# Optimization experiments

Measured on AMD Instinct MI355X. Metric: run time of the kernel, lower is better.

The kernel has to match this reference:

```python
import jax, jax.numpy as jnp
import numpy as np

DIM = 256
HEADS = 4
HEAD_DIM = DIM // HEADS
SCALE = HEAD_DIM ** -0.5


def setup_inputs() -> dict:
    key = jax.random.key(0)
    ks = jax.random.split(key, 6)
    B, N, C = 4, 2048, DIM
    t2_grad = jax.random.normal(ks[0], (B, N, C), dtype=jnp.float32)
    t1 = jax.random.normal(ks[1], (B, N, C), dtype=jnp.float32)
    # Linear weights stored as (in, out) so y = x @ W
    Wq = jax.random.normal(ks[2], (C, C), dtype=jnp.float32) * (C ** -0.5)
    Wkv = jax.random.normal(ks[3], (C, 2 * C), dtype=jnp.float32) * (C ** -0.5)
    Wproj = jax.random.normal(ks[4], (C, C), dtype=jnp.float32) * (C ** -0.5)
    bproj = jax.random.normal(ks[5], (C,), dtype=jnp.float32) * 0.01
    gamma = jnp.zeros((1,), dtype=jnp.float32)
    return {"t2_grad": t2_grad, "t1": t1, "Wq": Wq, "Wkv": Wkv,
            "Wproj": Wproj, "bproj": bproj, "gamma": gamma}


def lam(x, gamma):
    # x: (B, H, N, d) -> channel attention over d
    B, H, N, d = x.shape
    xp = jnp.transpose(x, (0, 3, 1, 2))            # (B, d, H, N)
    flat = xp.reshape(B, d, H * N)                 # (B, d, H*N)
    energy = jnp.einsum('bdm,bem->bde', flat, flat)  # (B, d, d)
    # Original applies softmax to raw energy (energy_new is discarded)
    attention = jax.nn.softmax(energy, axis=-1)
    out = jnp.einsum('bde,bem->bdm', attention, flat).reshape(B, d, H, N)
    out = gamma[0] * out + xp
    return jnp.transpose(out, (0, 2, 3, 1))        # (B, H, N, d)


def reference(t2_grad, t1, Wq, Wkv, Wproj, bproj, gamma):
    B, N, C = t2_grad.shape
    H, d = HEADS, HEAD_DIM
    q = (t2_grad @ Wq).reshape(B, N, H, d).transpose(0, 2, 1, 3)      # (B,H,N,d)
    kv = (t1 @ Wkv).reshape(B, N, 2, H, d).transpose(2, 0, 3, 1, 4)   # (2,B,H,N,d)
    k, v = kv[0], kv[1]
    attn = jax.nn.softmax(jnp.einsum('bhnd,bhmd->bhnm', q, k) * SCALE, axis=-1)
    x_other = jnp.einsum('bhnm,bhmd->bhnd', attn, v)                  # (B,H,N,d)
    x_other = lam(x_other, gamma)
    x_other = x_other.transpose(0, 2, 1, 3).reshape(B, N, C) \
        + q.transpose(0, 2, 1, 3).reshape(B, N, C)
    x = t2_grad + x_other
    return x @ Wproj + bproj
```

## Files before the change

kernel.cpp:

```cpp
#include <hip/hip_runtime.h>
#include <hip/hip_bf16.h>


typedef __attribute__((ext_vector_type(8))) short short8_t;
typedef __attribute__((ext_vector_type(4))) float f32x4;
typedef __attribute__((ext_vector_type(2))) unsigned u32x2;

#define NSEQ 2048

static __device__ __forceinline__ short f2bf(float f) {
  union { float f; unsigned u; } v; v.f = f;
  unsigned u = v.u;
  unsigned r = (u + 0x7FFFu + ((u >> 16) & 1u)) >> 16;
  return (short)r;
}
static __device__ __forceinline__ float bf2f(short s) {
  union { unsigned u; float f; } v;
  v.u = ((unsigned)(unsigned short)s) << 16;
  return v.f;
}
static __device__ __forceinline__ unsigned bcu(float f) {
  return __builtin_bit_cast(unsigned, f);
}
static __device__ __forceinline__ unsigned pkbf(float lo, float hi) {
  return __builtin_amdgcn_perm(bcu(hi), bcu(lo), 0x07060302u);
}
static __device__ __forceinline__ short f2bf_hw(float f) {
  __hip_bfloat16 h = __float2bfloat16(f);
  return __builtin_bit_cast(short, h);
}
static __device__ __forceinline__ unsigned pk2bf_hw(float a, float b) {
  return ((unsigned)(unsigned short)__builtin_bit_cast(short, __float2bfloat16(b)) << 16) |
         (unsigned short)__builtin_bit_cast(short, __float2bfloat16(a));
}
static __device__ __forceinline__ f32x4 vmax4(f32x4 a, f32x4 b) {
  f32x4 r;
  r[0] = fmaxf(a[0], b[0]); r[1] = fmaxf(a[1], b[1]);
  r[2] = fmaxf(a[2], b[2]); r[3] = fmaxf(a[3], b[3]);
  return r;
}

static __device__ __forceinline__ void gload_lds16(const short* src, short* ldst) {
  __builtin_amdgcn_global_load_lds(
      (const __attribute__((address_space(1))) unsigned*)src,
      (__attribute__((address_space(3))) unsigned*)ldst, 16, 0, 0);
}

__global__ __launch_bounds__(256) void wconv(
    const float* __restrict__ Wq, const float* __restrict__ Wkv,
    const float* __restrict__ Wp, short* __restrict__ Wqt,
    short* __restrict__ Wkvt, short* __restrict__ Wpt) {
  int tid = blockIdx.x * 256 + threadIdx.x;
  if (tid < 65536) {
    int n = tid >> 8, k = tid & 255;
    Wqt[tid] = f2bf(Wq[k * 256 + n]);
  } else if (tid < 196608) {
    int i = tid - 65536;
    int n = i >> 8, k = i & 255;
    Wkvt[i] = f2bf(Wkv[k * 512 + n]);
  } else {
    int i = tid - 196608;
    int n = i >> 8, k = i & 255;
    Wpt[i] = f2bf(Wp[k * 256 + n]);
  }
}

__global__ __launch_bounds__(256) void gemm_qkv3(
    const float* __restrict__ t2, const float* __restrict__ t1,
    const short* __restrict__ Wqt, const short* __restrict__ Wkvt,
    short* __restrict__ Qb, short* __restrict__ Kb, short* __restrict__ Vtb) {
  __shared__ __align__(16) short ldsA[32 * 256];
  int tid = threadIdx.x;
  int m0 = blockIdx.x * 32;
  int y = blockIdx.y;
  const float* A = (y == 0) ? t2 : t1;

  const float* ap = A + (size_t)m0 * 256;
#pragma unroll
  for (int i = 0; i < 8; i++) {
    int idx = i * 256 + tid;
    int row = idx >> 6, c4 = idx & 63;
    f32x4 v = *(const f32x4*)(ap + (size_t)idx * 4);
    int ch8 = c4 >> 1, half = c4 & 1;
    int swz = ch8 ^ (row & 7);
    unsigned* dst = (unsigned*)&ldsA[row * 256 + swz * 8 + half * 4];
    dst[0] = pk2bf_hw(v[0], v[1]);
    dst[1] = pk2bf_hw(v[2], v[3]);
  }
  __syncthreads();

  int w = tid >> 6, l = tid & 63, lr = l & 15, lg = l >> 4;
  short8_t af[2][8];
#pragma unroll
  for (int mt = 0; mt < 2; mt++)
#pragma unroll
    for (int ks = 0; ks < 8; ks++)
      af[mt][ks] = *(const short8_t*)&ldsA[(mt * 16 + lr) * 256 +
                                           (((ks * 4 + lg) ^ (lr & 7)) * 8)];

  const short* Bt = (y == 0) ? Wqt : (y == 1 ? Wkvt : Wkvt + 65536);
  f32x4 acc[2][4] = {};
#pragma unroll
  for (int ct = 0; ct < 4; ct++) {
    const short* br = Bt + (size_t)(w * 64 + ct * 16 + lr) * 256 + lg * 8;
    short8_t bfr[8];
#pragma unroll
    for (int ks = 0; ks < 8; ks++) bfr[ks] = *(const short8_t*)(br + ks * 32);
    if (y < 2) {
#pragma unroll
      for (int ks = 0; ks < 8; ks++) {
        acc[0][ct] = __builtin_amdgcn_mfma_f32_16x16x32_bf16(af[0][ks], bfr[ks], acc[0][ct], 0, 0, 0);
        acc[1][ct] = __builtin_amdgcn_mfma_f32_16x16x32_bf16(af[1][ks], bfr[ks], acc[1][ct], 0, 0, 0);
      }
    } else {
#pragma unroll
      for (int ks = 0; ks < 8; ks++) {
        acc[0][ct] = __builtin_amdgcn_mfma_f32_16x16x32_bf16(bfr[ks], af[0][ks], acc[0][ct], 0, 0, 0);
        acc[1][ct] = __builtin_amdgcn_mfma_f32_16x16x32_bf16(bfr[ks], af[1][ks], acc[1][ct], 0, 0, 0);
      }
    }
  }
  if (y < 2) {
    short* Ob = (y == 0) ? Qb : Kb;
#pragma unroll
    for (int ct = 0; ct < 4; ct++) {
      int c = w * 64 + ct * 16 + lr;
      int h = c >> 6, dd = c & 63;
#pragma unroll
      for (int mt = 0; mt < 2; mt++)
#pragma unroll
        for (int r = 0; r < 4; r++) {
          int m = m0 + mt * 16 + lg * 4 + r;
          int bb = m >> 11, n = m & 2047;
          Ob[(size_t)(((bb << 2) + h) * NSEQ + n) * 64 + dd] =
              f2bf_hw(acc[mt][ct][r]);
        }
    }
  } else {
#pragma unroll
    for (int ct = 0; ct < 4; ct++) {
      int c = w * 64 + ct * 16 + lg * 4;
#pragma unroll
      for (int mt = 0; mt < 2; mt++) {
        int m = m0 + mt * 16 + lr;
        int bb = m >> 11, n = m & 2047;
#pragma unroll
        for (int r = 0; r < 4; r++) {
          int cc = c + r;
          int h = cc >> 6, dd = cc & 63;
          Vtb[(size_t)(((bb << 2) + h) * 64 + dd) * NSEQ + n] =
              f2bf_hw(acc[mt][ct][r]);
        }
      }
    }
  }
}

template <int NS>
__global__ __launch_bounds__(256, 4) void flash_attn_split(
    const short* __restrict__ Qb, const short* __restrict__ Kb,
    const short* __restrict__ Vt, short* __restrict__ O0,
    short* __restrict__ O1, short* __restrict__ O2,
    short* __restrict__ O3, float* __restrict__ ML) {
  constexpr int KITER = 32 / NS;
  __shared__ __align__(16) short ldsK[2][4096];
  __shared__ __align__(16) short ldsV[4096];
  __shared__ __align__(16) short ldsP[4][2048];
  int tid = threadIdx.x;
  int w = tid >> 6, l = tid & 63, lr = l & 15, lg = l >> 4;
  int bh = blockIdx.y;
  int qt = blockIdx.x / NS, split = blockIdx.x % NS;
  int q0 = qt * 128 + w * 32;
  const short* qpA = Qb + ((size_t)bh * NSEQ + q0 + lr) * 64 + lg * 8;
  const short* qpB = qpA + 16 * 64;
  short8_t qfA0 = *(const short8_t*)qpA;
  short8_t qfA1 = *(const short8_t*)(qpA + 32);
  short8_t qfB0 = *(const short8_t*)qpB;
  short8_t qfB1 = *(const short8_t*)(qpB + 32);
  const short* kbase = Kb + (size_t)bh * NSEQ * 64;
  const short* vbase = Vt + (size_t)bh * 64 * NSEQ;

  int r0 = tid >> 3, ch0 = (tid & 7) ^ (r0 & 7);
  int kb0 = split * KITER;
  const short* ksrc = kbase + (size_t)kb0 * 4096 + (size_t)r0 * 64 + ch0 * 8;
  const short* vsrc = vbase + (size_t)r0 * NSEQ + kb0 * 64 + ch0 * 8;
  short* ldKw0 = &ldsK[0][0] + w * 512;
  short* ldKw1 = &ldsK[1][0] + w * 512;
  short* ldVw = &ldsV[0] + w * 512;

#define STAGE_K(dst_, it_)                                  \
  {                                                         \
    const short* s_ = ksrc + (size_t)(it_) * 4096;          \
    gload_lds16(s_, dst_);                                  \
    gload_lds16(s_ + 2048, (dst_) + 2048);                  \
  }
#define STAGE_V(it_)                                        \
  {                                                         \
    const short* s_ = vsrc + (size_t)(it_) * 64;            \
    gload_lds16(s_, ldVw);                                  \
    gload_lds16(s_ + 32 * NSEQ, ldVw + 2048);               \
  }

  f32x4 oA[4] = {}, oB[4] = {};
  float osumA = 0.f, osumB = 0.f, m2A = -1e30f, m2B = -1e30f;
  const float C = 0.125f * 1.44269504089f;

  int sw = lr & 7;
  int rdA = (lg ^ sw) * 8;
  int rdB = ((lg + 4) ^ sw) * 8;
  short* Pw = &ldsP[w][0];
  short* wrA = Pw + lr * 64 + (lg & 1) * 4;
  short* wrB = wrA + 16 * 64;
  int chhi = lg >> 1;
  const short* prA0 = Pw + lr * 64 + (lg ^ sw) * 8;
  const short* prA1 = Pw + lr * 64 + ((4 + lg) ^ sw) * 8;
  const short* prB0 = prA0 + 16 * 64;
  const short* prB1 = prA1 + 16 * 64;

  STAGE_K(ldKw0, 0);

  for (int i = 0; i < KITER; i++) {
    asm volatile("s_waitcnt vmcnt(0)" ::: "memory");
    __builtin_amdgcn_s_barrier();
    STAGE_V(i);
    if (i + 1 < KITER) {
      short* d_ = (i & 1) ? ldKw0 : ldKw1;
      STAGE_K(d_, i + 1);
    }
    const short* lK = (i & 1) ? &ldsK[1][0] : &ldsK[0][0];
    f32x4 sA[4], sB[4];
    __builtin_amdgcn_s_setprio(1);
#pragma unroll
    for (int t = 0; t < 4; t++) {
      const short* kr = lK + (t * 16 + lr) * 64;
      short8_t kf0 = *(const short8_t*)(kr + rdA);
      short8_t kf1 = *(const short8_t*)(kr + rdB);
      f32x4 z = {0.f, 0.f, 0.f, 0.f};
      f32x4 zA = __builtin_amdgcn_mfma_f32_16x16x32_bf16(kf0, qfA0, z, 0, 0, 0);
      sA[t] = __builtin_amdgcn_mfma_f32_16x16x32_bf16(kf1, qfA1, zA, 0, 0, 0);
      f32x4 zB = __builtin_amdgcn_mfma_f32_16x16x32_bf16(kf0, qfB0, z, 0, 0, 0);
      sB[t] = __builtin_amdgcn_mfma_f32_16x16x32_bf16(kf1, qfB1, zB, 0, 0, 0);
    }
    __builtin_amdgcn_s_setprio(0);
    f32x4 mA4 = vmax4(vmax4(sA[0], sA[1]), vmax4(sA[2], sA[3]));
    f32x4 mB4 = vmax4(vmax4(sB[0], sB[1]), vmax4(sB[2], sB[3]));
    float mxA = fmaxf(fmaxf(mA4[0], mA4[1]), fmaxf(mA4[2], mA4[3]));
    float mxB = fmaxf(fmaxf(mB4[0], mB4[1]), fmaxf(mB4[2], mB4[3]));
    mxA = fmaxf(mxA, __shfl_xor(mxA, 16));
    mxA = fmaxf(mxA, __shfl_xor(mxA, 32));
    mxB = fmaxf(mxB, __shfl_xor(mxB, 16));
    mxB = fmaxf(mxB, __shfl_xor(mxB, 32));
    mxA *= C;
    mxB *= C;
    float mnA = fmaxf(m2A, mxA), mnB = fmaxf(m2B, mxB);
    if (__any(fmaxf(mnA - m2A, mnB - m2B) > 8.f)) {
      float aA = __builtin_amdgcn_exp2f(m2A - mnA);
      float aB = __builtin_amdgcn_exp2f(m2B - mnB);
      m2A = mnA; m2B = mnB;
      osumA *= aA; osumB *= aB;
#pragma unroll
      for (int dt = 0; dt < 4; dt++) { oA[dt] *= aA; oB[dt] *= aB; }
    }
    float psA = 0.f, psB = 0.f;
#pragma unroll
    for (int t = 0; t < 4; t++) {
      float a0 = __builtin_amdgcn_exp2f(__builtin_fmaf(sA[t][0], C, -m2A));
      float a1 = __builtin_amdgcn_exp2f(__builtin_fmaf(sA[t][1], C, -m2A));
      float a2 = __builtin_amdgcn_exp2f(__builtin_fmaf(sA[t][2], C, -m2A));
      float a3 = __builtin_amdgcn_exp2f(__builtin_fmaf(sA[t][3], C, -m2A));
      psA += (a0 + a1) + (a2 + a3);
      u32x2 ua = {pkbf(a0, a1), pkbf(a2, a3)};
      *(u32x2*)(wrA + ((2 * t + chhi) ^ sw) * 8) = ua;
      float b0 = __builtin_amdgcn_exp2f(__builtin_fmaf(sB[t][0], C, -m2B));
      float b1 = __builtin_amdgcn_exp2f(__builtin_fmaf(sB[t][1], C, -m2B));
      float b2 = __builtin_amdgcn_exp2f(__builtin_fmaf(sB[t][2], C, -m2B));
      float b3 = __builtin_amdgcn_exp2f(__builtin_fmaf(sB[t][3], C, -m2B));
      psB += (b0 + b1) + (b2 + b3);
      u32x2 ub = {pkbf(b0, b1), pkbf(b2, b3)};
      *(u32x2*)(wrB + ((2 * t + chhi) ^ sw) * 8) = ub;
    }
    osumA += psA;
    osumB += psB;
    short8_t pA0 = *(const short8_t*)prA0;
    short8_t pA1 = *(const short8_t*)prA1;
    short8_t pB0 = *(const short8_t*)prB0;
    short8_t pB1 = *(const short8_t*)prB1;
    if (i + 1 < KITER)
      asm volatile("s_waitcnt vmcnt(2)" ::: "memory");
    else
      asm volatile("s_waitcnt vmcnt(0)" ::: "memory");
    __builtin_amdgcn_s_barrier();
    __builtin_amdgcn_s_setprio(1);
#pragma unroll
    for (int dt = 0; dt < 4; dt++) {
      const short* vr = &ldsV[0] + (dt * 16 + lr) * 64;
      short8_t vf0 = *(const short8_t*)(vr + rdA);
      short8_t vf1 = *(const short8_t*)(vr + rdB);
      oA[dt] = __builtin_amdgcn_mfma_f32_16x16x32_bf16(vf0, pA0, oA[dt], 0, 0, 0);
      oA[dt] = __builtin_amdgcn_mfma_f32_16x16x32_bf16(vf1, pA1, oA[dt], 0, 0, 0);
      oB[dt] = __builtin_amdgcn_mfma_f32_16x16x32_bf16(vf0, pB0, oB[dt], 0, 0, 0);
      oB[dt] = __builtin_amdgcn_mfma_f32_16x16x32_bf16(vf1, pB1, oB[dt], 0, 0, 0);
    }
    __builtin_amdgcn_s_setprio(0);
  }
#undef STAGE_K
#undef STAGE_V
  osumA += __shfl_xor(osumA, 16);
  osumA += __shfl_xor(osumA, 32);
  osumB += __shfl_xor(osumB, 16);
  osumB += __shfl_xor(osumB, 32);
  float invA = __builtin_amdgcn_rcpf(osumA);
  float invB = __builtin_amdgcn_rcpf(osumB);
  short* op = (split == 0) ? O0 : (split == 1) ? O1 : (split == 2) ? O2 : O3;
#pragma unroll
  for (int dt = 0; dt < 4; dt++)
#pragma unroll
    for (int r = 0; r < 4; r++) {
      size_t drow = ((size_t)bh * 64 + dt * 16 + lg * 4 + r) * NSEQ;
      op[drow + q0 + lr] = f2bf_hw(oA[dt][r] * invA);
      op[drow + q0 + 16 + lr] = f2bf_hw(oB[dt][r] * invB);
    }
  if (lg == 0) {
    float2 vA = {m2A, osumA};
    float2 vB = {m2B, osumB};
    *(float2*)&ML[((size_t)bh * NSEQ + q0 + lr) * 8 + split * 2] = vA;
    *(float2*)&ML[((size_t)bh * NSEQ + q0 + 16 + lr) * 8 + split * 2] = vB;
  }
}

template <int NS>
__global__ __launch_bounds__(256) void combine_xf(
    const short* __restrict__ O0, const short* __restrict__ O1,
    const short* __restrict__ O2, const short* __restrict__ O3,
    const float* __restrict__ ML, const float* __restrict__ gamma,
    const float* __restrict__ t2, const short* __restrict__ Qb,
    short* __restrict__ AOb, float* __restrict__ partials,
    short* __restrict__ Xf) {
  __shared__ __align__(16) short tileT[64][128];
  __shared__ f32x4 wcol[128];
  int tid = threadIdx.x;
  int b = blockIdx.y, kc = blockIdx.x;
  int h = kc >> 4, n0 = (kc & 15) * 128;
  int bh = (b << 2) + h;
  float g = gamma[0];
  if (tid < 128) {
    const float* ml = ML + ((size_t)bh * NSEQ + n0 + tid) * 8;
    f32x4 a = *(const f32x4*)ml;
    f32x4 c;
    if (NS == 2) {
      float M = fmaxf(a[0], a[2]);
      float w0 = a[1] * __builtin_amdgcn_exp2f(a[0] - M);
      float w1 = a[3] * __builtin_amdgcn_exp2f(a[2] - M);
      float iv = __builtin_amdgcn_rcpf(w0 + w1);
      c[0] = w0 * iv; c[1] = w1 * iv; c[2] = 0.f; c[3] = 0.f;
    } else {
      f32x4 bq = *(const f32x4*)(ml + 4);
      float M = fmaxf(fmaxf(a[0], a[2]), fmaxf(bq[0], bq[2]));
      float w0 = a[1] * __builtin_amdgcn_exp2f(a[0] - M);
      float w1 = a[3] * __builtin_amdgcn_exp2f(a[2] - M);
      float w2 = bq[1] * __builtin_amdgcn_exp2f(bq[0] - M);
      float w3 = bq[3] * __builtin_amdgcn_exp2f(bq[2] - M);
      float iv = __builtin_amdgcn_rcpf(w0 + w1 + w2 + w3);
      c[0] = w0 * iv; c[1] = w1 * iv; c[2] = w2 * iv; c[3] = w3 * iv;
    }
    wcol[tid] = c;
  }
  __syncthreads();
  {
    int chunk = tid & 15;
    int rw = tid >> 4;
#pragma unroll
    for (int i = 0; i < 4; i++) {
      int row = rw + 16 * i;
      size_t gbase = ((size_t)bh * 64 + row) * NSEQ + n0 + chunk * 8;
      short8_t v0 = *(const short8_t*)(O0 + gbase);
      short8_t v1 = *(const short8_t*)(O1 + gbase);
      short8_t v2{}, v3{};
      if (NS == 4) {
        v2 = *(const short8_t*)(O2 + gbase);
        v3 = *(const short8_t*)(O3 + gbase);
      }
      short8_t comb;
#pragma unroll
      for (int j = 0; j < 8; j++) {
        f32x4 c = wcol[chunk * 8 + j];
        float val = bf2f(v0[j]) * c[0] + bf2f(v1[j]) * c[1];
        if (NS == 4) val += bf2f(v2[j]) * c[2] + bf2f(v3[j]) * c[3];
        comb[j] = f2bf_hw(val);
      }
      if (g != 0.f) *(short8_t*)(AOb + gbase) = comb;
      *(short8_t*)&tileT[row][(chunk ^ (row & 15)) * 8] = comb;
    }
  }
  __syncthreads();
  if (g == 0.f) {
    int nc = tid >> 1, half = tid & 1;
    int n = n0 + nc;
    int cidx = nc >> 3, jj = nc & 7;
    const float* t2p = t2 + ((size_t)b * NSEQ + n) * 256 + h * 64 + half * 32;
    const short* qp = Qb + ((size_t)bh * NSEQ + n) * 64 + half * 32;
    short* xfp = Xf + ((size_t)b * NSEQ + n) * 256 + h * 64 + half * 32;
#pragma unroll
    for (int i = 0; i < 4; i++) {
      int ddb = half * 32 + i * 8;
      f32x4 ta = *(const f32x4*)(t2p + i * 8);
      f32x4 tb = *(const f32x4*)(t2p + i * 8 + 4);
      short8_t q8 = *(const short8_t*)(qp + i * 8);
      short8_t r;
#pragma unroll
      for (int j = 0; j < 8; j++) {
        int dd = ddb + j;
        short xv = tileT[dd][((cidx ^ (dd & 15)) * 8) + jj];
        float t = (j < 4) ? ta[j] : tb[j - 4];
        r[j] = f2bf_hw(t + bf2f(xv) + bf2f(q8[j]));
      }
      *(short8_t*)(xfp + i * 8) = r;
    }
    return;
  }
  int w = tid >> 6, lr = tid & 15, lg = (tid & 63) >> 4;
  f32x4 acc[4] = {};
#pragma unroll
  for (int ks = 0; ks < 4; ks++) {
    short8_t af = *(const short8_t*)&tileT[w * 16 + lr][((ks * 4 + lg) ^ lr) * 8];
#pragma unroll
    for (int e = 0; e < 4; e++) {
      short8_t bf = *(const short8_t*)&tileT[e * 16 + lr][((ks * 4 + lg) ^ lr) * 8];
      acc[e] = __builtin_amdgcn_mfma_f32_16x16x32_bf16(af, bf, acc[e], 0, 0, 0);
    }
  }
  float* dst = partials + ((size_t)b * 64 + kc) * 4096;
#pragma unroll
  for (int e = 0; e < 4; e++)
#pragma unroll
    for (int r = 0; r < 4; r++)
      dst[(w * 16 + lg * 4 + r) * 64 + e * 16 + lr] = acc[e][r];
}

__global__ __launch_bounds__(64) void energy_reduce_softmax(
    const float* __restrict__ partials, const float* __restrict__ gamma,
    float* __restrict__ attnc) {
  if (gamma[0] == 0.f) return;
  int row = blockIdx.x;
  int b = row >> 6, d = row & 63;
  int e = threadIdx.x;
  const float* src = partials + (size_t)b * 64 * 4096 + d * 64 + e;
  float s = 0.f;
#pragma unroll 8
  for (int kc = 0; kc < 64; kc++) s += src[(size_t)kc * 4096];
  float mx = s;
#pragma unroll
  for (int x = 1; x < 64; x <<= 1) mx = fmaxf(mx, __shfl_xor(mx, x, 64));
  float ev = __expf(s - mx);
  float sum = ev;
#pragma unroll
  for (int x = 1; x < 64; x <<= 1) sum += __shfl_xor(sum, x, 64);
  attnc[row * 64 + e] = ev / sum;
}

__global__ __launch_bounds__(256) void assemble_x(
    const short* __restrict__ AOb, const float* __restrict__ attnc,
    const float* __restrict__ t2, const short* __restrict__ Qb,
    const float* __restrict__ gamma, short* __restrict__ Xf) {
  float g = gamma[0];
  if (g == 0.f) return;
  __shared__ f32x4 At4[1024];
  int b = blockIdx.y, tid = threadIdx.x;
  const f32x4* ac = (const f32x4*)(attnc + (size_t)b * 4096);
#pragma unroll
  for (int i = 0; i < 4; i++) At4[i * 256 + tid] = ac[i * 256 + tid];
  __syncthreads();
  int rowb = blockIdx.x * 256 + tid;
  int h = rowb >> 11, n = rowb & 2047;
  const short* xop = AOb + ((size_t)((b << 2) + h) * 64) * NSEQ + n;
  f32x4 xv[16];
#pragma unroll
  for (int i = 0; i < 16; i++) {
    f32x4 t;
    t[0] = bf2f(xop[(size_t)(4 * i + 0) * NSEQ]);
    t[1] = bf2f(xop[(size_t)(4 * i + 1) * NSEQ]);
    t[2] = bf2f(xop[(size_t)(4 * i + 2) * NSEQ]);
    t[3] = bf2f(xop[(size_t)(4 * i + 3) * NSEQ]);
    xv[i] = t;
  }
  const short* qp = Qb + ((size_t)b * 8192 + rowb) * 64;
  const float* t2p = t2 + ((size_t)b * 2048 + n) * 256 + h * 64;
  short* xfp = Xf + ((size_t)b * 2048 + n) * 256 + h * 64;
#pragma unroll
  for (int dd = 0; dd < 64; dd++) {
    f32x4 a = {0.f, 0.f, 0.f, 0.f};
#pragma unroll
    for (int j = 0; j < 16; j++) a += At4[dd * 16 + j] * xv[j];
    float o = (a[0] + a[1] + a[2] + a[3]) * g;
    float val = t2p[dd] + o + xv[dd >> 2][dd & 3] + bf2f(qp[dd]);
    xfp[dd] = f2bf(val);
  }
}

__global__ __launch_bounds__(256) void gemm_proj(
    const short* __restrict__ Xf, const short* __restrict__ Wpt,
    const float* __restrict__ bias, float* __restrict__ out) {
  __shared__ __align__(16) short ldsA[16 * 256];
  int tid = threadIdx.x;
  int w = tid >> 6, l = tid & 63, lr = l & 15, lg = l >> 4;
  int m0 = blockIdx.x * 16;
#pragma unroll
  for (int i = 0; i < 2; i++) {
    int c = w * 128 + i * 64 + l;
    int row = c >> 5, ch = c & 31;
    int chs = (ch & 24) | ((ch & 7) ^ (row & 7));
    gload_lds16(Xf + (size_t)(m0 + row) * 256 + chs * 8,
                &ldsA[(w * 128 + i * 64) * 8]);
  }
  asm volatile("s_waitcnt vmcnt(0)" ::: "memory");
  __syncthreads();
  short8_t af[8];
#pragma unroll
  for (int ks = 0; ks < 8; ks++)
    af[ks] = *(const short8_t*)&ldsA[lr * 256 + (((ks * 4 + lg) ^ (lr & 7)) * 8)];
  f32x4 acc[4] = {};
#pragma unroll
  for (int ct = 0; ct < 4; ct++) {
    const short* br = Wpt + (size_t)(w * 64 + ct * 16 + lr) * 256 + lg * 8;
    short8_t bfr[8];
#pragma unroll
    for (int ks = 0; ks < 8; ks++) bfr[ks] = *(const short8_t*)(br + ks * 32);
#pragma unroll
    for (int ks = 0; ks < 8; ks++)
      acc[ct] = __builtin_amdgcn_mfma_f32_16x16x32_bf16(af[ks], bfr[ks], acc[ct], 0, 0, 0);
  }
#pragma unroll
  for (int ct = 0; ct < 4; ct++) {
    int c = w * 64 + ct * 16 + lr;
    float bc = bias[c];
#pragma unroll
    for (int r = 0; r < 4; r++) {
      int m = m0 + lg * 4 + r;
      out[(size_t)m * 256 + c] = acc[ct][r] + bc;
    }
  }
}

extern "C" void kernel_launch(void* const* d_in, const int* in_sizes, int n_in,
                              void* d_out, int out_size, void* d_ws, size_t ws_size,
                              hipStream_t stream) {
  const float* t2 = (const float*)d_in[0];
  const float* t1 = (const float*)d_in[1];
  const float* Wq = (const float*)d_in[2];
  const float* Wkv = (const float*)d_in[3];
  const float* Wp = (const float*)d_in[4];
  const float* bproj = (const float*)d_in[5];
  const float* gamma = (const float*)d_in[6];
  float* out = (float*)d_out;
  char* ws = (char*)d_ws;

  const size_t MB = 1024ull * 1024ull;
  short* Qb = (short*)(ws + 0);
  short* Kb = (short*)(ws + 4 * MB);
  float* partials = (float*)(ws + 4 * MB);
  short* Vt = (short*)(ws + 8 * MB);
  short* AOb = (short*)(ws + 8 * MB);
  short* Xf = (short*)(ws + 12 * MB);
  short* O0 = (short*)(ws + 16 * MB);
  short* O1 = (short*)(ws + 20 * MB);
  short* Wqt = (short*)(ws + 24 * MB);
  short* Wkvt = (short*)(ws + 24 * MB + 128 * 1024);
  short* Wpt = (short*)(ws + 24 * MB + 384 * 1024);
  float* attnc = (float*)(ws + 24 * MB + 512 * 1024);
  float* ML = (float*)(ws + 24 * MB + 576 * 1024);
  short* O2 = (short*)(ws + 26 * MB);
  short* O3 = (short*)(ws + 30 * MB);

  bool big = ws_size >= 34 * MB;

  wconv<<<1024, 256, 0, stream>>>(Wq, Wkv, Wp, Wqt, Wkvt, Wpt);
  gemm_qkv3<<<dim3(256, 3), 256, 0, stream>>>(t2, t1, Wqt, Wkvt, Qb, Kb, Vt);
  if (big) {
    flash_attn_split<4><<<dim3(64, 16), 256, 0, stream>>>(Qb, Kb, Vt, O0, O1,
                                                          O2, O3, ML);
    combine_xf<4><<<dim3(64, 4), 256, 0, stream>>>(
        O0, O1, O2, O3, ML, gamma, t2, Qb, AOb, partials, Xf);
  } else {
    flash_attn_split<2><<<dim3(32, 16), 256, 0, stream>>>(Qb, Kb, Vt, O0, O1,
                                                          O1, O1, ML);
    combine_xf<2><<<dim3(64, 4), 256, 0, stream>>>(
        O0, O1, O1, O1, ML, gamma, t2, Qb, AOb, partials, Xf);
  }
  energy_reduce_softmax<<<256, 64, 0, stream>>>(partials, gamma, attnc);
  assemble_x<<<dim3(32, 4), 256, 0, stream>>>(AOb, attnc, t2, Qb, gamma, Xf);
  gemm_proj<<<512, 256, 0, stream>>>(Xf, Wpt, bproj, out);
}
```

Before: 78.56 us.

## Double-buffer V with K and process A/B query halves sequentially

Double-buffers the V tile alongside K so both are prefetched one iteration ahead, cutting the barriers per iteration from two to one. The two 16-row query sub-tiles are now handled one after the other: each runs softmax, writes P into a halved per-wave LDS buffer, then does its PV MFMAs. This reuses the P buffer and lets the softmax of one half overlap the MFMAs of the other. LDS use stays the same (V doubled, P halved), and reusing the single P buffer per wave depends on in-order LDS accesses within a wave.

```diff
diff --git a/kernel.cpp b/kernel.cpp
--- a/kernel.cpp
+++ b/kernel.cpp
@@ -164,8 +164,8 @@
     short* __restrict__ O3, float* __restrict__ ML) {
   constexpr int KITER = 32 / NS;
   __shared__ __align__(16) short ldsK[2][4096];
-  __shared__ __align__(16) short ldsV[4096];
-  __shared__ __align__(16) short ldsP[4][2048];
+  __shared__ __align__(16) short ldsV[2][4096];
+  __shared__ __align__(16) short ldsP[4][1024];
   int tid = threadIdx.x;
   int w = tid >> 6, l = tid & 63, lr = l & 15, lg = l >> 4;
   int bh = blockIdx.y;
@@ -186,19 +186,19 @@
   const short* vsrc = vbase + (size_t)r0 * NSEQ + kb0 * 64 + ch0 * 8;
   short* ldKw0 = &ldsK[0][0] + w * 512;
   short* ldKw1 = &ldsK[1][0] + w * 512;
-  short* ldVw = &ldsV[0] + w * 512;
-
-#define STAGE_K(dst_, it_)                                  \
+  short* ldVw0 = &ldsV[0][0] + w * 512;
+  short* ldVw1 = &ldsV[1][0] + w * 512;
+
+#define STAGE_KV(buf_, it_)                                 \
   {                                                         \
-    const short* s_ = ksrc + (size_t)(it_) * 4096;          \
-    gload_lds16(s_, dst_);                                  \
-    gload_lds16(s_ + 2048, (dst_) + 2048);                  \
-  }
-#define STAGE_V(it_)                                        \
-  {                                                         \
-    const short* s_ = vsrc + (size_t)(it_) * 64;            \
-    gload_lds16(s_, ldVw);                                  \
-    gload_lds16(s_ + 32 * NSEQ, ldVw + 2048);               \
+    const short* sk_ = ksrc + (size_t)(it_) * 4096;         \
+    short* dk_ = (buf_) ? ldKw1 : ldKw0;                    \
+    gload_lds16(sk_, dk_);                                  \
+    gload_lds16(sk_ + 2048, dk_ + 2048);                    \
+    const short* sv_ = vsrc + (size_t)(it_) * 64;           \
+    short* dv_ = (buf_) ? ldVw1 : ldVw0;                    \
+    gload_lds16(sv_, dv_);                                  \
+    gload_lds16(sv_ + 32 * NSEQ, dv_ + 2048);               \
   }
 
   f32x4 oA[4] = {}, oB[4] = {};
@@ -209,25 +209,20 @@
   int rdA = (lg ^ sw) * 8;
   int rdB = ((lg + 4) ^ sw) * 8;
   short* Pw = &ldsP[w][0];
-  short* wrA = Pw + lr * 64 + (lg & 1) * 4;
-  short* wrB = wrA + 16 * 64;
+  short* wrP = Pw + lr * 64 + (lg & 1) * 4;
   int chhi = lg >> 1;
-  const short* prA0 = Pw + lr * 64 + (lg ^ sw) * 8;
-  const short* prA1 = Pw + lr * 64 + ((4 + lg) ^ sw) * 8;
-  const short* prB0 = prA0 + 16 * 64;
-  const short* prB1 = prA1 + 16 * 64;
-
-  STAGE_K(ldKw0, 0);
+  const short* pr0 = Pw + lr * 64 + (lg ^ sw) * 8;
+  const short* pr1 = Pw + lr * 64 + ((4 + lg) ^ sw) * 8;
+
+  STAGE_KV(0, 0);
+  asm volatile("s_waitcnt vmcnt(0)" ::: "memory");
+  __builtin_amdgcn_s_barrier();
 
   for (int i = 0; i < KITER; i++) {
-    asm volatile("s_waitcnt vmcnt(0)" ::: "memory");
-    __builtin_amdgcn_s_barrier();
-    STAGE_V(i);
-    if (i + 1 < KITER) {
-      short* d_ = (i & 1) ? ldKw0 : ldKw1;
-      STAGE_K(d_, i + 1);
-    }
-    const short* lK = (i & 1) ? &ldsK[1][0] : &ldsK[0][0];
+    int buf = i & 1;
+    if (i + 1 < KITER) STAGE_KV(buf ^ 1, i + 1);
+    const short* lK = buf ? &ldsK[1][0] : &ldsK[0][0];
+    const short* lV = buf ? &ldsV[1][0] : &ldsV[0][0];
     f32x4 sA[4], sB[4];
     __builtin_amdgcn_s_setprio(1);
 #pragma unroll
@@ -242,69 +237,90 @@
       sB[t] = __builtin_amdgcn_mfma_f32_16x16x32_bf16(kf1, qfB1, zB, 0, 0, 0);
     }
     __builtin_amdgcn_s_setprio(0);
-    f32x4 mA4 = vmax4(vmax4(sA[0], sA[1]), vmax4(sA[2], sA[3]));
-    f32x4 mB4 = vmax4(vmax4(sB[0], sB[1]), vmax4(sB[2], sB[3]));
-    float mxA = fmaxf(fmaxf(mA4[0], mA4[1]), fmaxf(mA4[2], mA4[3]));
-    float mxB = fmaxf(fmaxf(mB4[0], mB4[1]), fmaxf(mB4[2], mB4[3]));
-    mxA = fmaxf(mxA, __shfl_xor(mxA, 16));
-    mxA = fmaxf(mxA, __shfl_xor(mxA, 32));
-    mxB = fmaxf(mxB, __shfl_xor(mxB, 16));
-    mxB = fmaxf(mxB, __shfl_xor(mxB, 32));
-    mxA *= C;
-    mxB *= C;
-    float mnA = fmaxf(m2A, mxA), mnB = fmaxf(m2B, mxB);
-    if (__any(fmaxf(mnA - m2A, mnB - m2B) > 8.f)) {
-      float aA = __builtin_amdgcn_exp2f(m2A - mnA);
-      float aB = __builtin_amdgcn_exp2f(m2B - mnB);
-      m2A = mnA; m2B = mnB;
-      osumA *= aA; osumB *= aB;
-#pragma unroll
-      for (int dt = 0; dt < 4; dt++) { oA[dt] *= aA; oB[dt] *= aB; }
-    }
-    float psA = 0.f, psB = 0.f;
-#pragma unroll
-    for (int t = 0; t < 4; t++) {
-      float a0 = __builtin_amdgcn_exp2f(__builtin_fmaf(sA[t][0], C, -m2A));
-      float a1 = __builtin_amdgcn_exp2f(__builtin_fmaf(sA[t][1], C, -m2A));
-      float a2 = __builtin_amdgcn_exp2f(__builtin_fmaf(sA[t][2], C, -m2A));
-      float a3 = __builtin_amdgcn_exp2f(__builtin_fmaf(sA[t][3], C, -m2A));
-      psA += (a0 + a1) + (a2 + a3);
-      u32x2 ua = {pkbf(a0, a1), pkbf(a2, a3)};
-      *(u32x2*)(wrA + ((2 * t + chhi) ^ sw) * 8) = ua;
-      float b0 = __builtin_amdgcn_exp2f(__builtin_fmaf(sB[t][0], C, -m2B));
-      float b1 = __builtin_amdgcn_exp2f(__builtin_fmaf(sB[t][1], C, -m2B));
-      float b2 = __builtin_amdgcn_exp2f(__builtin_fmaf(sB[t][2], C, -m2B));
-      float b3 = __builtin_amdgcn_exp2f(__builtin_fmaf(sB[t][3], C, -m2B));
-      psB += (b0 + b1) + (b2 + b3);
-      u32x2 ub = {pkbf(b0, b1), pkbf(b2, b3)};
-      *(u32x2*)(wrB + ((2 * t + chhi) ^ sw) * 8) = ub;
-    }
-    osumA += psA;
-    osumB += psB;
-    short8_t pA0 = *(const short8_t*)prA0;
-    short8_t pA1 = *(const short8_t*)prA1;
-    short8_t pB0 = *(const short8_t*)prB0;
-    short8_t pB1 = *(const short8_t*)prB1;
-    if (i + 1 < KITER)
-      asm volatile("s_waitcnt vmcnt(2)" ::: "memory");
-    else
+    {
+      f32x4 m4 = vmax4(vmax4(sA[0], sA[1]), vmax4(sA[2], sA[3]));
+      float mx = fmaxf(fmaxf(m4[0], m4[1]), fmaxf(m4[2], m4[3]));
+      mx = fmaxf(mx, __shfl_xor(mx, 16));
+      mx = fmaxf(mx, __shfl_xor(mx, 32));
+      mx *= C;
+      float mn = fmaxf(m2A, mx);
+      if (__any(mn - m2A > 8.f)) {
+        float a = __builtin_amdgcn_exp2f(m2A - mn);
+        m2A = mn;
+        osumA *= a;
+#pragma unroll
+        for (int dt = 0; dt < 4; dt++) oA[dt] *= a;
+      }
+      float ps = 0.f;
+#pragma unroll
+      for (int t = 0; t < 4; t++) {
+        float p0 = __builtin_amdgcn_exp2f(__builtin_fmaf(sA[t][0], C, -m2A));
+        float p1 = __builtin_amdgcn_exp2f(__builtin_fmaf(sA[t][1], C, -m2A));
+        float p2 = __builtin_amdgcn_exp2f(__builtin_fmaf(sA[t][2], C, -m2A));
+        float p3 = __builtin_amdgcn_exp2f(__builtin_fmaf(sA[t][3], C, -m2A));
+        ps += (p0 + p1) + (p2 + p3);
+        u32x2 u = {pkbf(p0, p1), pkbf(p2, p3)};
+        *(u32x2*)(wrP + ((2 * t + chhi) ^ sw) * 8) = u;
+      }
+      osumA += ps;
+      short8_t pf0 = *(const short8_t*)pr0;
+      short8_t pf1 = *(const short8_t*)pr1;
+      __builtin_amdgcn_s_setprio(1);
+#pragma unroll
+      for (int dt = 0; dt < 4; dt++) {
+        const short* vr = lV + (dt * 16 + lr) * 64;
+        short8_t vf0 = *(const short8_t*)(vr + rdA);
+        short8_t vf1 = *(const short8_t*)(vr + rdB);
+        oA[dt] = __builtin_amdgcn_mfma_f32_16x16x32_bf16(vf0, pf0, oA[dt], 0, 0, 0);
+        oA[dt] = __builtin_amdgcn_mfma_f32_16x16x32_bf16(vf1, pf1, oA[dt], 0, 0, 0);
+      }
+      __builtin_amdgcn_s_setprio(0);
+    }
+    {
+      f32x4 m4 = vmax4(vmax4(sB[0], sB[1]), vmax4(sB[2], sB[3]));
+      float mx = fmaxf(fmaxf(m4[0], m4[1]), fmaxf(m4[2], m4[3]));
+      mx = fmaxf(mx, __shfl_xor(mx, 16));
+      mx = fmaxf(mx, __shfl_xor(mx, 32));
+      mx *= C;
+      float mn = fmaxf(m2B, mx);
+      if (__any(mn - m2B > 8.f)) {
+        float a = __builtin_amdgcn_exp2f(m2B - mn);
+        m2B = mn;
+        osumB *= a;
+#pragma unroll
+        for (int dt = 0; dt < 4; dt++) oB[dt] *= a;
+      }
+      float ps = 0.f;
+#pragma unroll
+      for (int t = 0; t < 4; t++) {
+        float p0 = __builtin_amdgcn_exp2f(__builtin_fmaf(sB[t][0], C, -m2B));
+        float p1 = __builtin_amdgcn_exp2f(__builtin_fmaf(sB[t][1], C, -m2B));
+        float p2 = __builtin_amdgcn_exp2f(__builtin_fmaf(sB[t][2], C, -m2B));
+        float p3 = __builtin_amdgcn_exp2f(__builtin_fmaf(sB[t][3], C, -m2B));
+        ps += (p0 + p1) + (p2 + p3);
+        u32x2 u = {pkbf(p0, p1), pkbf(p2, p3)};
+        *(u32x2*)(wrP + ((2 * t + chhi) ^ sw) * 8) = u;
+      }
+      osumB += ps;
+      short8_t pf0 = *(const short8_t*)pr0;
+      short8_t pf1 = *(const short8_t*)pr1;
+      __builtin_amdgcn_s_setprio(1);
+#pragma unroll
+      for (int dt = 0; dt < 4; dt++) {
+        const short* vr = lV + (dt * 16 + lr) * 64;
+        short8_t vf0 = *(const short8_t*)(vr + rdA);
+        short8_t vf1 = *(const short8_t*)(vr + rdB);
+        oB[dt] = __builtin_amdgcn_mfma_f32_16x16x32_bf16(vf0, pf0, oB[dt], 0, 0, 0);
+        oB[dt] = __builtin_amdgcn_mfma_f32_16x16x32_bf16(vf1, pf1, oB[dt], 0, 0, 0);
+      }
+      __builtin_amdgcn_s_setprio(0);
+    }
+    if (i + 1 < KITER) {
       asm volatile("s_waitcnt vmcnt(0)" ::: "memory");
-    __builtin_amdgcn_s_barrier();
-    __builtin_amdgcn_s_setprio(1);
-#pragma unroll
-    for (int dt = 0; dt < 4; dt++) {
-      const short* vr = &ldsV[0] + (dt * 16 + lr) * 64;
-      short8_t vf0 = *(const short8_t*)(vr + rdA);
-      short8_t vf1 = *(const short8_t*)(vr + rdB);
-      oA[dt] = __builtin_amdgcn_mfma_f32_16x16x32_bf16(vf0, pA0, oA[dt], 0, 0, 0);
-      oA[dt] = __builtin_amdgcn_mfma_f32_16x16x32_bf16(vf1, pA1, oA[dt], 0, 0, 0);
-      oB[dt] = __builtin_amdgcn_mfma_f32_16x16x32_bf16(vf0, pB0, oB[dt], 0, 0, 0);
-      oB[dt] = __builtin_amdgcn_mfma_f32_16x16x32_bf16(vf1, pB1, oB[dt], 0, 0, 0);
-    }
-    __builtin_amdgcn_s_setprio(0);
-  }
-#undef STAGE_K
-#undef STAGE_V
+      __builtin_amdgcn_s_barrier();
+    }
+  }
+#undef STAGE_KV
   osumA += __shfl_xor(osumA, 16);
   osumA += __shfl_xor(osumA, 32);
   osumB += __shfl_xor(osumB, 16);
```

New measurement: 77.83 us. No clear change (-0.9%).
